# Kernel optimization log

Measured on AMD Instinct MI355X. Metric: run time of the kernel, lower is better.

Reference implementation:

```python
import jax, jax.numpy as jnp
import numpy as np

N_RBF = 20
CUTOFF = 5.0
N_BASIS = 128
N_FILTERS = 128
N_LAYERS = 3
B, N = 128, 128
N_PAIRS = 524288


def ssp(x):
    # ShiftedSoftplus: softplus(x) - log(2)
    return jax.nn.softplus(x) - jnp.log(2.0).astype(x.dtype)


def gaussian_rbf(d):
    # schnetpack-style GaussianRBF: offsets in [0, cutoff], shared width
    offsets = jnp.linspace(0.0, CUTOFF, N_RBF, dtype=d.dtype)
    width = offsets[1] - offsets[0]
    coeff = -0.5 / (width * width)
    diff = d[:, None] - offsets[None, :]  # [n_pairs, n_rbf]
    return jnp.exp(coeff * diff * diff)


def cosine_cutoff(d):
    fc = 0.5 * (jnp.cos(d * (jnp.pi / CUTOFF)) + 1.0)
    return fc * (d < CUTOFF).astype(d.dtype)


def setup_inputs() -> dict:
    key = jax.random.key(0)
    ks = jax.random.split(key, 16)
    inp = {
        "Z": jax.random.randint(ks[0], (B, N), 0, 100),
        "R": jax.random.normal(ks[1], (B, N, 3), dtype=jnp.float32) * 2.0,
        "idx_i": jax.random.randint(ks[2], (N_PAIRS,), 0, B * N),
        "idx_j": jax.random.randint(ks[3], (N_PAIRS,), 0, B * N),
        "emb": jax.random.normal(ks[4], (100, N_BASIS), dtype=jnp.float32) * 0.1,
    }
    s = 0.05
    inp["in2f_W"] = jax.random.normal(ks[5], (N_LAYERS, N_BASIS, N_FILTERS), dtype=jnp.float32) * s
    inp["in2f_b"] = jnp.zeros((N_LAYERS, N_FILTERS), dtype=jnp.float32)
    inp["fW1"] = jax.random.normal(ks[6], (N_LAYERS, N_RBF, N_FILTERS), dtype=jnp.float32) * s
    inp["fb1"] = jnp.zeros((N_LAYERS, N_FILTERS), dtype=jnp.float32)
    inp["fW2"] = jax.random.normal(ks[7], (N_LAYERS, N_FILTERS, N_FILTERS), dtype=jnp.float32) * s
    inp["fb2"] = jnp.zeros((N_LAYERS, N_FILTERS), dtype=jnp.float32)
    inp["oW1"] = jax.random.normal(ks[8], (N_LAYERS, N_FILTERS, N_BASIS), dtype=jnp.float32) * s
    inp["ob1"] = jnp.zeros((N_LAYERS, N_BASIS), dtype=jnp.float32)
    inp["oW2"] = jax.random.normal(ks[9], (N_LAYERS, N_BASIS, N_BASIS), dtype=jnp.float32) * s
    inp["ob2"] = jnp.zeros((N_LAYERS, N_BASIS), dtype=jnp.float32)
    return inp


def _interaction(x, f_ij, rcut_ij, idx_i, idx_j, W_in, b_in, fW1, fb1, fW2, fb2, oW1, ob1, oW2, ob2):
    # x: [B, N, n_atom_basis]
    h = jnp.einsum("bnf,fg->bng", x, W_in) + b_in          # input_to_feature
    h = h.reshape(-1, h.shape[-1])                           # [B*N, n_filters]
    # filter network on RBFs
    Wij = ssp(f_ij @ fW1 + fb1) @ fW2 + fb2                  # [n_pairs, n_filters]
    Wij = Wij * rcut_ij[:, None]
    x_ij = h[idx_j] * Wij                                     # gather + multiply
    agg = jax.ops.segment_sum(x_ij, idx_i, num_segments=h.shape[0])  # scatter_add
    out = ssp(agg @ oW1 + ob1) @ oW2 + ob2                    # feature_to_output
    return out.reshape(x.shape[0], x.shape[1], N_BASIS)


def reference(Z, R, idx_i, idx_j, emb, in2f_W, in2f_b, fW1, fb1, fW2, fb2, oW1, ob1, oW2, ob2):
    coords = R.reshape(-1, 3)                                 # [B*N, 3]
    vec = coords[idx_i] - coords[idx_j]
    d_ij = jnp.linalg.norm(vec, axis=-1)                      # [n_pairs]
    f_ij = gaussian_rbf(d_ij)                                 # [n_pairs, 20]
    rcut_ij = cosine_cutoff(d_ij)                             # [n_pairs]
    x = emb[Z]                                                # [B, N, 128]
    for l in range(N_LAYERS):
        v = _interaction(x, f_ij, rcut_ij, idx_i, idx_j,
                         in2f_W[l], in2f_b[l], fW1[l], fb1[l], fW2[l], fb2[l],
                         oW1[l], ob1[l], oW2[l], ob2[l])
        x = x + v
    return x
```

## Files before the change

### kernel.cpp

```cpp
#include <hip/hip_runtime.h>
#include <hip/hip_fp16.h>

#define NPAIRS 524288
#define NATOMS 16384
#define TBINS  2048
#define TROWS  2049
#define CAP    80
#define CUTOFF_F 5.0f

#define MB_G0    256
#define MB_TAB   (MB_G0 + 771)
#define MB_WC    (MB_TAB + 72)
#define MB_TOTAL (MB_WC + 2048)

typedef _Float16 f16;
typedef f16 f16x4 __attribute__((ext_vector_type(4)));
typedef f16 f16x8 __attribute__((ext_vector_type(8)));
typedef float f32x4 __attribute__((ext_vector_type(4)));

__device__ __forceinline__ float sspf(float v) {
  float a = fabsf(v);
  return fmaxf(v, 0.0f) + log1pf(expf(-a)) - 0.69314718055994531f;
}

__device__ __forceinline__ int swz(int row, int kh) {
  return (row << 8) + ((kh << 1) ^ ((row & 7) << 4));
}
__device__ __forceinline__ int swzW(int col, int kh) {
  return (col << 7) + ((kh << 1) ^ ((col & 7) << 4));
}
__device__ __forceinline__ f16x8 ldW(const f16* __restrict__ Wg, int col, int ss, int hi) {
  return *(const f16x8*)((const char*)Wg + (ss >> 1) * 16384 + swzW(col, (ss & 1) * 32 + hi * 8));
}

__device__ __forceinline__ uint4 ldtab(const f16* __restrict__ tabL, int v, int c) {
  return *(const uint4*)(tabL + ((unsigned)(v >> 14) << 7) + (c << 3));
}
__device__ __forceinline__ uint4 ldh(const f16* __restrict__ hin, int v, int c) {
  return *(const uint4*)(hin + ((unsigned)(v & 16383) << 7) + (c << 3));
}
__device__ __forceinline__ void dot8(float* acc, uint4 wv, uint4 hv) {
  const __half* wp = (const __half*)&wv;
  const __half* hp = (const __half*)&hv;
  #pragma unroll
  for (int q = 0; q < 8; ++q)
    acc[q] = fmaf(__half2float(wp[q]), __half2float(hp[q]), acc[q]);
}

__global__ __launch_bounds__(256) void zero_kernel(int* __restrict__ p) {
  p[blockIdx.x * 256 + threadIdx.x] = 0;
}

__global__ __launch_bounds__(256) void mega(const int* __restrict__ Z,
                                            const float* __restrict__ emb,
                                            const float* __restrict__ in2f_W,
                                            const float* __restrict__ in2f_b,
                                            const float* __restrict__ fW1,
                                            const float* __restrict__ fb1,
                                            const float* __restrict__ fW2,
                                            const float* __restrict__ fb2,
                                            const float* __restrict__ oW1,
                                            const float* __restrict__ oW2,
                                            const int* __restrict__ idx_i,
                                            const int* __restrict__ idx_j,
                                            const float* __restrict__ R,
                                            f16* __restrict__ table,
                                            f16* __restrict__ wsw,
                                            int* __restrict__ cursor,
                                            int* __restrict__ pjd,
                                            f16* __restrict__ hout) {
  __shared__ char smem[16384];
  int t = threadIdx.x;
  int bid = blockIdx.x;

  if (bid < MB_G0) {
    char* Wl = smem;
    size_t rbase = (size_t)bid * 64;
    int w = t >> 6, lane = t & 63;
    int lo = lane & 15, hi = lane >> 4;

    int z = Z[rbase + 16 * w + lo];
    const float* erow = emb + (size_t)z * 128;
    f16x8 fa[4];
    #pragma unroll
    for (int ss = 0; ss < 4; ++ss) {
      float4 a = *(const float4*)(erow + ss * 32 + hi * 8);
      float4 b = *(const float4*)(erow + ss * 32 + hi * 8 + 4);
      f16x8 v = { (f16)a.x, (f16)a.y, (f16)a.z, (f16)a.w,
                  (f16)b.x, (f16)b.y, (f16)b.z, (f16)b.w };
      fa[ss] = v;
    }

    f32x4 acc[8];
    #pragma unroll
    for (int cb = 0; cb < 8; ++cb) acc[cb] = (f32x4){0.0f, 0.0f, 0.0f, 0.0f};

    #pragma unroll
    for (int h = 0; h < 2; ++h) {
      #pragma unroll
      for (int i = 0; i < 4; ++i) {
        int tloc = i * 256 + t;
        int col = tloc & 127, kc = tloc >> 7;
        f16x8 v;
        #pragma unroll
        for (int kk = 0; kk < 8; ++kk)
          v[kk] = (f16)in2f_W[(h * 64 + kc * 8 + kk) * 128 + col];
        *(f16x8*)(Wl + swzW(col, kc * 8)) = v;
      }
      __syncthreads();
      #pragma unroll
      for (int cb = 0; cb < 8; ++cb) {
        int col = cb * 16 + lo;
        #pragma unroll
        for (int sh = 0; sh < 2; ++sh) {
          f16x8 fb = *(f16x8*)(Wl + swzW(col, sh * 32 + hi * 8));
          acc[cb] = __builtin_amdgcn_mfma_f32_16x16x32_f16(fa[h * 2 + sh], fb, acc[cb], 0, 0, 0);
        }
      }
      __syncthreads();
    }

    #pragma unroll
    for (int cb = 0; cb < 8; ++cb) {
      int col = cb * 16 + lo;
      float bc = in2f_b[col];
      #pragma unroll
      for (int j = 0; j < 4; ++j)
        hout[(rbase + 16 * w + hi * 4 + j) * 128 + col] = (f16)(acc[cb][j] + bc);
    }
    return;
  }

  if (bid < MB_TAB) {
    float* hid = (float*)smem;
    int bid2 = bid - MB_G0;
    int l = bid2 / 257, rem = bid2 % 257;
    int e = t >> 5, q = t & 31;
    int ti = rem * 8 + e;
    const float* W1 = fW1 + (size_t)l * 20 * 128;
    const float* B1 = fb1 + (size_t)l * 128;
    const float* W2 = fW2 + (size_t)l * 128 * 128;
    const float* B2 = fb2 + (size_t)l * 128;

    const float width = CUTOFF_F / 19.0f;
    const float coeff = -0.5f / (width * width);
    const float dstep = CUTOFF_F / (float)TBINS;
    float d = (float)ti * dstep;

    float4 h4 = *(const float4*)&B1[q * 4];
    #pragma unroll
    for (int r = 0; r < 20; ++r) {
      float diff = d - (float)r * width;
      float fr = expf(coeff * diff * diff);
      float4 w4 = *(const float4*)&W1[r * 128 + q * 4];
      h4.x += fr * w4.x; h4.y += fr * w4.y; h4.z += fr * w4.z; h4.w += fr * w4.w;
    }
    *(float4*)&hid[e * 128 + q * 4] =
        make_float4(sspf(h4.x), sspf(h4.y), sspf(h4.z), sspf(h4.w));
    __syncthreads();

    float4 o4 = *(const float4*)&B2[q * 4];
    const float4* W2g = (const float4*)W2;
    #pragma unroll 4
    for (int g = 0; g < 128; ++g) {
      float hv = hid[e * 128 + g];
      float4 w4 = W2g[g * 32 + q];
      o4.x += hv * w4.x; o4.y += hv * w4.y; o4.z += hv * w4.z; o4.w += hv * w4.w;
    }

    if (ti < TROWS) {
      float fc = (d < CUTOFF_F) ? 0.5f * (cosf(d * 0.62831853071795865f) + 1.0f) : 0.0f;
      f16x4 hv = { (f16)(o4.x * fc), (f16)(o4.y * fc), (f16)(o4.z * fc), (f16)(o4.w * fc) };
      *(f16x4*)((f16*)table + ((size_t)l * TROWS + ti) * 128 + q * 4) = hv;
    }
    return;
  }

  if (bid < MB_WC) {
    int bid2 = bid - MB_TAB;
    int mm = bid2 >> 3;
    int tloc = (bid2 & 7) * 256 + t;
    int col = tloc & 127, k0 = (tloc >> 7) << 3;
    const float* src = mm < 3 ? in2f_W + (size_t)mm * 16384
                     : mm < 6 ? oW1 + (size_t)(mm - 3) * 16384
                              : oW2 + (size_t)(mm - 6) * 16384;
    f16x8 v;
    #pragma unroll
    for (int kk = 0; kk < 8; ++kk) v[kk] = (f16)src[(k0 + kk) * 128 + col];
    *(f16x8*)((char*)wsw + (size_t)mm * 32768 + (k0 >> 6) * 16384 + swzW(col, k0 & 63)) = v;
    return;
  }

  {
    int p = (bid - MB_WC) * 256 + t;
    int i = idx_i[p], j = idx_j[p];
    float dx = R[(size_t)i*3+0] - R[(size_t)j*3+0];
    float dy = R[(size_t)i*3+1] - R[(size_t)j*3+1];
    float dz = R[(size_t)i*3+2] - R[(size_t)j*3+2];
    float d = sqrtf(dx*dx + dy*dy + dz*dz);
    if (d < CUTOFF_F) {
      int bin = __float2int_rn(d * ((float)TBINS / CUTOFF_F));
      int slot = atomicAdd(&cursor[i], 1);
      if (slot < CAP) pjd[i * CAP + slot] = j | (bin << 14);
    }
  }
}

template <int FIRST, int HAS_NEXT>
__global__ __launch_bounds__(512, 8) void aggfuse(const int* __restrict__ pjd,
                                                  const int* __restrict__ cnt,
                                                  const f16* __restrict__ hin,
                                                  const f16* __restrict__ tabL,
                                                  const f16* __restrict__ W1g,
                                                  const float* __restrict__ ob1,
                                                  const f16* __restrict__ W2g,
                                                  const float* __restrict__ ob2,
                                                  const int* __restrict__ Z,
                                                  const float* __restrict__ emb,
                                                  float* __restrict__ x,
                                                  const f16* __restrict__ Wng,
                                                  const float* __restrict__ bn,
                                                  f16* __restrict__ hout) {
  __shared__ char smem[8192];
  char* AlT = smem;
  char* Tl  = smem + 4096;
  int tid = threadIdx.x;
  int wv = tid >> 6, lane = tid & 63;
  int s = lane >> 4, c = lane & 15;
  int rbase = blockIdx.x * 16;
  const int S = (TBINS << 14);

  {
    int a = rbase + wv * 2 + (s & 1);
    int half = s >> 1;
    int p0 = a * CAP;
    int n = min(cnt[a], CAP);
    int nh = half * 2;

    int m = (n + 3) >> 2;
    m = max(m, __shfl_xor(m, 16, 64));
    m = max(m, __shfl_xor(m, 32, 64));

    float acc[8];
    #pragma unroll
    for (int q = 0; q < 8; ++q) acc[q] = 0.0f;

    int vA  = (nh < n)     ? pjd[p0 + nh]     : S;
    int vB  = (nh + 1 < n) ? pjd[p0 + nh + 1] : S;
    int vA1 = (nh + 4 < n) ? pjd[p0 + nh + 4] : S;
    int vB1 = (nh + 5 < n) ? pjd[p0 + nh + 5] : S;
    uint4 wA = ldtab(tabL, vA, c), hA = ldh(hin, vA, c);
    uint4 wB = ldtab(tabL, vB, c), hB = ldh(hin, vB, c);

    for (int it = 0; it < m; ++it) {
      int k2 = 4 * (it + 2) + nh;
      int vA2 = (k2 < n)     ? pjd[p0 + k2]     : S;
      int vB2 = (k2 + 1 < n) ? pjd[p0 + k2 + 1] : S;
      uint4 wAn = ldtab(tabL, vA1, c), hAn = ldh(hin, vA1, c);
      uint4 wBn = ldtab(tabL, vB1, c), hBn = ldh(hin, vB1, c);
      dot8(acc, wA, hA);
      dot8(acc, wB, hB);
      wA = wAn; hA = hAn; wB = wBn; hB = hBn;
      vA1 = vA2; vB1 = vB2;
    }

    #pragma unroll
    for (int q = 0; q < 8; ++q) acc[q] += __shfl_xor(acc[q], 32, 64);

    if (s < 2) {
      int row = wv * 2 + s;
      f16x8 pk;
      #pragma unroll
      for (int q = 0; q < 8; ++q) pk[q] = (f16)acc[q];
      *(f16x8*)(AlT + swz(row, c * 8)) = pk;
    }
  }
  __syncthreads();

  int lo = c, hi = s;
  int col = wv * 16 + lo;

  float res[4];
  if (FIRST) {
    #pragma unroll
    for (int j = 0; j < 4; ++j) {
      int z = Z[rbase + hi * 4 + j];
      res[j] = emb[(size_t)z * 128 + col];
    }
  } else {
    #pragma unroll
    for (int j = 0; j < 4; ++j)
      res[j] = x[(size_t)(rbase + hi * 4 + j) * 128 + col];
  }

  {
    f32x4 acc = {0.0f, 0.0f, 0.0f, 0.0f};
    #pragma unroll
    for (int ss = 0; ss < 4; ++ss) {
      f16x8 fa = *(f16x8*)(AlT + swz(lo, ss * 32 + hi * 8));
      acc = __builtin_amdgcn_mfma_f32_16x16x32_f16(fa, ldW(W1g, col, ss, hi), acc, 0, 0, 0);
    }
    float bc = ob1[col];
    #pragma unroll
    for (int j = 0; j < 4; ++j)
      *(f16*)(Tl + swz(hi * 4 + j, col)) = (f16)sspf(acc[j] + bc);
  }
  __syncthreads();

  {
    f32x4 acc = {0.0f, 0.0f, 0.0f, 0.0f};
    #pragma unroll
    for (int ss = 0; ss < 4; ++ss) {
      f16x8 fa = *(f16x8*)(Tl + swz(lo, ss * 32 + hi * 8));
      acc = __builtin_amdgcn_mfma_f32_16x16x32_f16(fa, ldW(W2g, col, ss, hi), acc, 0, 0, 0);
    }
    float bc = ob2[col];
    #pragma unroll
    for (int j = 0; j < 4; ++j) {
      int r = hi * 4 + j;
      float xn = res[j] + acc[j] + bc;
      x[(size_t)(rbase + r) * 128 + col] = xn;
      if (HAS_NEXT) *(f16*)(AlT + swz(r, col)) = (f16)xn;
    }
  }

  if (HAS_NEXT) {
    __syncthreads();
    f32x4 acc = {0.0f, 0.0f, 0.0f, 0.0f};
    #pragma unroll
    for (int ss = 0; ss < 4; ++ss) {
      f16x8 fa = *(f16x8*)(AlT + swz(lo, ss * 32 + hi * 8));
      acc = __builtin_amdgcn_mfma_f32_16x16x32_f16(fa, ldW(Wng, col, ss, hi), acc, 0, 0, 0);
    }
    float bc = bn[col];
    #pragma unroll
    for (int j = 0; j < 4; ++j)
      hout[(size_t)(rbase + hi * 4 + j) * 128 + col] = (f16)(acc[j] + bc);
  }
}

extern "C" void kernel_launch(void* const* d_in, const int* in_sizes, int n_in,
                              void* d_out, int out_size, void* d_ws, size_t ws_size,
                              hipStream_t stream) {
  const int*   Z      = (const int*)d_in[0];
  const float* R      = (const float*)d_in[1];
  const int*   idx_i  = (const int*)d_in[2];
  const int*   idx_j  = (const int*)d_in[3];
  const float* emb    = (const float*)d_in[4];
  const float* in2f_W = (const float*)d_in[5];
  const float* in2f_b = (const float*)d_in[6];
  const float* fW1    = (const float*)d_in[7];
  const float* fb1    = (const float*)d_in[8];
  const float* fW2    = (const float*)d_in[9];
  const float* fb2    = (const float*)d_in[10];
  const float* oW1    = (const float*)d_in[11];
  const float* ob1    = (const float*)d_in[12];
  const float* oW2    = (const float*)d_in[13];
  const float* ob2    = (const float*)d_in[14];
  float* x = (float*)d_out;

  char* ws = (char*)d_ws;
  int*  cursor = (int*) (ws + 0x000000);
  int*  pjd    = (int*) (ws + 0x010000);
  f16*  table  = (f16*) (ws + 0x510000);
  f16*  h0     = (f16*) (ws + 0x6A0000);
  f16*  h1     = (f16*) (ws + 0xAA0000);
  f16*  wsw    = (f16*) (ws + 0xEA0000);

  zero_kernel<<<NATOMS / 256, 256, 0, stream>>>(cursor);
  mega<<<MB_TOTAL, 256, 0, stream>>>(Z, emb, in2f_W, in2f_b, fW1, fb1, fW2, fb2,
                                     oW1, oW2, idx_i, idx_j, R,
                                     table, wsw, cursor, pjd, h0);

  aggfuse<1, 1><<<NATOMS / 16, 512, 0, stream>>>(pjd, cursor, h0, table + 0 * (size_t)TROWS * 128,
                                                 wsw + 3 * 16384, ob1,
                                                 wsw + 6 * 16384, ob2,
                                                 Z, emb, x,
                                                 wsw + 1 * 16384, in2f_b + 128, h1);
  aggfuse<0, 1><<<NATOMS / 16, 512, 0, stream>>>(pjd, cursor, h1, table + 1 * (size_t)TROWS * 128,
                                                 wsw + 4 * 16384, ob1 + 128,
                                                 wsw + 7 * 16384, ob2 + 128,
                                                 Z, emb, x,
                                                 wsw + 2 * 16384, in2f_b + 256, h0);
  aggfuse<0, 0><<<NATOMS / 16, 512, 0, stream>>>(pjd, cursor, h0, table + 2 * (size_t)TROWS * 128,
                                                 wsw + 5 * 16384, ob1 + 256,
                                                 wsw + 8 * 16384, ob2 + 256,
                                                 Z, emb, x, nullptr, nullptr, nullptr);
}
```

Measured before the change: 111.1 us.

## Halve filter table resolution and compute table rows with MFMA

The precomputed distance-to-filter lookup table is cut from 2048 to 1024 bins. Its second dense layer is now a 16-row f16 MFMA tile per block, with W2 staged into swizzled shared memory, replacing scalar fp32 FMAs over 8 rows. Fewer table blocks and tensor-core math are meant to shorten the setup stage, and a smaller table may cache better in the gather phase. The trade is coarser distance interpolation and f16 rounding of the hidden activations, which could affect accuracy.

```diff
diff --git a/kernel.cpp b/kernel.cpp
--- a/kernel.cpp
+++ b/kernel.cpp
@@ -3,13 +3,14 @@
 
 #define NPAIRS 524288
 #define NATOMS 16384
-#define TBINS  2048
-#define TROWS  2049
+#define TBINS  1024
+#define TROWS  1025
 #define CAP    80
 #define CUTOFF_F 5.0f
 
+#define NTBL     65
 #define MB_G0    256
-#define MB_TAB   (MB_G0 + 771)
+#define MB_TAB   (MB_G0 + 3 * NTBL)
 #define MB_WC    (MB_TAB + 72)
 #define MB_TOTAL (MB_WC + 2048)
 
@@ -69,7 +70,7 @@
                                             int* __restrict__ cursor,
                                             int* __restrict__ pjd,
                                             f16* __restrict__ hout) {
-  __shared__ char smem[16384];
+  __shared__ char smem[20480];
   int t = threadIdx.x;
   int bid = blockIdx.x;
 
@@ -132,46 +133,91 @@
   }
 
   if (bid < MB_TAB) {
-    float* hid = (float*)smem;
+    char* Al = smem;
+    char* Wl = smem + 4096;
     int bid2 = bid - MB_G0;
-    int l = bid2 / 257, rem = bid2 % 257;
-    int e = t >> 5, q = t & 31;
-    int ti = rem * 8 + e;
+    int l = bid2 / NTBL, rem = bid2 % NTBL;
+    int e16 = rem * 16;
     const float* W1 = fW1 + (size_t)l * 20 * 128;
     const float* B1 = fb1 + (size_t)l * 128;
     const float* W2 = fW2 + (size_t)l * 128 * 128;
     const float* B2 = fb2 + (size_t)l * 128;
-
     const float width = CUTOFF_F / 19.0f;
     const float coeff = -0.5f / (width * width);
     const float dstep = CUTOFF_F / (float)TBINS;
-    float d = (float)ti * dstep;
-
-    float4 h4 = *(const float4*)&B1[q * 4];
-    #pragma unroll
-    for (int r = 0; r < 20; ++r) {
-      float diff = d - (float)r * width;
-      float fr = expf(coeff * diff * diff);
-      float4 w4 = *(const float4*)&W1[r * 128 + q * 4];
-      h4.x += fr * w4.x; h4.y += fr * w4.y; h4.z += fr * w4.z; h4.w += fr * w4.w;
-    }
-    *(float4*)&hid[e * 128 + q * 4] =
-        make_float4(sspf(h4.x), sspf(h4.y), sspf(h4.z), sspf(h4.w));
+
+    {
+      int e = t >> 4, q = t & 15;
+      float d = (float)(e16 + e) * dstep;
+      float rbf[20];
+      #pragma unroll
+      for (int r = 0; r < 20; ++r) {
+        float diff = d - (float)r * width;
+        rbf[r] = expf(coeff * diff * diff);
+      }
+      float4 hA = *(const float4*)&B1[q * 8];
+      float4 hB = *(const float4*)&B1[q * 8 + 4];
+      #pragma unroll
+      for (int r = 0; r < 20; ++r) {
+        float4 wa = *(const float4*)&W1[r * 128 + q * 8];
+        float4 wb = *(const float4*)&W1[r * 128 + q * 8 + 4];
+        hA.x += rbf[r] * wa.x; hA.y += rbf[r] * wa.y;
+        hA.z += rbf[r] * wa.z; hA.w += rbf[r] * wa.w;
+        hB.x += rbf[r] * wb.x; hB.y += rbf[r] * wb.y;
+        hB.z += rbf[r] * wb.z; hB.w += rbf[r] * wb.w;
+      }
+      f16x8 hv = { (f16)sspf(hA.x), (f16)sspf(hA.y), (f16)sspf(hA.z), (f16)sspf(hA.w),
+                   (f16)sspf(hB.x), (f16)sspf(hB.y), (f16)sspf(hB.z), (f16)sspf(hB.w) };
+      *(f16x8*)(Al + swz(e, q * 8)) = hv;
+    }
     __syncthreads();
 
-    float4 o4 = *(const float4*)&B2[q * 4];
-    const float4* W2g = (const float4*)W2;
-    #pragma unroll 4
-    for (int g = 0; g < 128; ++g) {
-      float hv = hid[e * 128 + g];
-      float4 w4 = W2g[g * 32 + q];
-      o4.x += hv * w4.x; o4.y += hv * w4.y; o4.z += hv * w4.z; o4.w += hv * w4.w;
-    }
-
-    if (ti < TROWS) {
-      float fc = (d < CUTOFF_F) ? 0.5f * (cosf(d * 0.62831853071795865f) + 1.0f) : 0.0f;
-      f16x4 hv = { (f16)(o4.x * fc), (f16)(o4.y * fc), (f16)(o4.z * fc), (f16)(o4.w * fc) };
-      *(f16x4*)((f16*)table + ((size_t)l * TROWS + ti) * 128 + q * 4) = hv;
+    int w = t >> 6, lane = t & 63;
+    int lo = lane & 15, hi = lane >> 4;
+    f32x4 acc[2];
+    acc[0] = (f32x4){0.0f, 0.0f, 0.0f, 0.0f};
+    acc[1] = (f32x4){0.0f, 0.0f, 0.0f, 0.0f};
+
+    #pragma unroll
+    for (int halfk = 0; halfk < 2; ++halfk) {
+      #pragma unroll
+      for (int i = 0; i < 4; ++i) {
+        int tloc = i * 256 + t;
+        int col = tloc & 127, kc = tloc >> 7;
+        f16x8 v;
+        #pragma unroll
+        for (int kk = 0; kk < 8; ++kk)
+          v[kk] = (f16)W2[(halfk * 64 + kc * 8 + kk) * 128 + col];
+        *(f16x8*)(Wl + swzW(col, kc * 8)) = v;
+      }
+      __syncthreads();
+      #pragma unroll
+      for (int cb = 0; cb < 2; ++cb) {
+        int col = (w * 2 + cb) * 16 + lo;
+        #pragma unroll
+        for (int sh = 0; sh < 2; ++sh) {
+          int ss = halfk * 2 + sh;
+          f16x8 fa = *(f16x8*)(Al + swz(lo, ss * 32 + hi * 8));
+          f16x8 fb = *(f16x8*)(Wl + swzW(col, sh * 32 + hi * 8));
+          acc[cb] = __builtin_amdgcn_mfma_f32_16x16x32_f16(fa, fb, acc[cb], 0, 0, 0);
+        }
+      }
+      __syncthreads();
+    }
+
+    #pragma unroll
+    for (int cb = 0; cb < 2; ++cb) {
+      int col = (w * 2 + cb) * 16 + lo;
+      float bc = B2[col];
+      #pragma unroll
+      for (int j = 0; j < 4; ++j) {
+        int ti = e16 + hi * 4 + j;
+        if (ti < TROWS) {
+          float d = (float)ti * dstep;
+          float fc = (d < CUTOFF_F) ? 0.5f * (cosf(d * 0.62831853071795865f) + 1.0f) : 0.0f;
+          ((f16*)table)[((size_t)l * TROWS + ti) * 128 + col] = (f16)((acc[cb][j] + bc) * fc);
+        }
+      }
     }
     return;
   }
@@ -233,7 +279,7 @@
   {
     int a = rbase + wv * 2 + (s & 1);
     int half = s >> 1;
-    int p0 = a * CAP;
+    const int* pp = pjd + a * CAP;
     int n = min(cnt[a], CAP);
     int nh = half * 2;
 
@@ -245,17 +291,17 @@
     #pragma unroll
     for (int q = 0; q < 8; ++q) acc[q] = 0.0f;
 
-    int vA  = (nh < n)     ? pjd[p0 + nh]     : S;
-    int vB  = (nh + 1 < n) ? pjd[p0 + nh + 1] : S;
-    int vA1 = (nh + 4 < n) ? pjd[p0 + nh + 4] : S;
-    int vB1 = (nh + 5 < n) ? pjd[p0 + nh + 5] : S;
+    int vA  = (nh     < n) ? pp[nh]     : S;
+    int vB  = (nh + 1 < n) ? pp[nh + 1] : S;
+    int vA1 = (nh + 4 < n) ? pp[nh + 4] : S;
+    int vB1 = (nh + 5 < n) ? pp[nh + 5] : S;
     uint4 wA = ldtab(tabL, vA, c), hA = ldh(hin, vA, c);
     uint4 wB = ldtab(tabL, vB, c), hB = ldh(hin, vB, c);
 
     for (int it = 0; it < m; ++it) {
       int k2 = 4 * (it + 2) + nh;
-      int vA2 = (k2 < n)     ? pjd[p0 + k2]     : S;
-      int vB2 = (k2 + 1 < n) ? pjd[p0 + k2 + 1] : S;
+      int vA2 = (k2 < n)     ? pp[k2]     : S;
+      int vB2 = (k2 + 1 < n) ? pp[k2 + 1] : S;
       uint4 wAn = ldtab(tabL, vA1, c), hAn = ldh(hin, vA1, c);
       uint4 wBn = ldtab(tabL, vB1, c), hBn = ldh(hin, vB1, c);
       dot8(acc, wA, hA);
@@ -362,10 +408,10 @@
   char* ws = (char*)d_ws;
   int*  cursor = (int*) (ws + 0x000000);
   int*  pjd    = (int*) (ws + 0x010000);
-  f16*  table  = (f16*) (ws + 0x510000);
-  f16*  h0     = (f16*) (ws + 0x6A0000);
-  f16*  h1     = (f16*) (ws + 0xAA0000);
-  f16*  wsw    = (f16*) (ws + 0xEA0000);
+  f16*  table  = (f16*) (ws + 0x520000);
+  f16*  h0     = (f16*) (ws + 0x600000);
+  f16*  h1     = (f16*) (ws + 0xA00000);
+  f16*  wsw    = (f16*) (ws + 0xE00000);
 
   zero_kernel<<<NATOMS / 256, 256, 0, stream>>>(cursor);
   mega<<<MB_TOTAL, 256, 0, stream>>>(Z, emb, in2f_W, in2f_b, fW1, fb1, fW2, fb2,
```

After: 101.5 us, median of 2. -8.6%, faster.
